# Kernel tuning notes

Measured on AMD Instinct MI355X. Metric: run time of the kernel, lower is better.

## Reference

```python
import jax, jax.numpy as jnp
import numpy as np

V, H, B, T = 32000, 1024, 64, 512
EPS = 1e-5


def setup_inputs() -> dict:
    key = jax.random.key(0)
    ks = jax.random.split(key, 12)
    s = lambda i, shape: (jax.random.normal(ks[i], shape, dtype=jnp.float32) * 0.02)
    inp = {
        "x": jax.random.randint(ks[0], (B, T), 0, V),
        "t": jax.random.uniform(ks[1], (B,), dtype=jnp.float32),
        "emb": s(2, (V, H)),
        "w_ih1": s(3, (4 * H, H)), "w_hh1": s(4, (4 * H, H)),
        "b_ih1": jnp.zeros((4 * H,), jnp.float32), "b_hh1": jnp.zeros((4 * H,), jnp.float32),
        "gamma1": jnp.ones((H,), jnp.float32), "beta1": jnp.zeros((H,), jnp.float32),
        "w_ih2": s(5, (4 * H, H)), "w_hh2": s(6, (4 * H, H)),
        "b_ih2": jnp.zeros((4 * H,), jnp.float32), "b_hh2": jnp.zeros((4 * H,), jnp.float32),
        "gamma2": jnp.ones((H,), jnp.float32), "beta2": jnp.zeros((H,), jnp.float32),
        "fc_w": s(7, (1, H)), "fc_b": jnp.zeros((1,), jnp.float32),
        # LockedDropout: one mask per layer, reused at every timestep, pre-scaled by 1/keep
        "mask1": jax.random.bernoulli(ks[8], 0.5, (B, H)).astype(jnp.float32) / 0.5,
        "mask2": jax.random.bernoulli(ks[9], 0.7, (B, H)).astype(jnp.float32) / 0.7,
    }
    return inp


def _lstm_step(xt, h, c, w_ih, w_hh, b_ih, b_hh):
    # PyTorch LSTMCell gate order: i, f, g, o
    g = xt @ w_ih.T + h @ w_hh.T + (b_ih + b_hh)
    i, f, gg, o = jnp.split(g, 4, axis=-1)
    c = jax.nn.sigmoid(f) * c + jax.nn.sigmoid(i) * jnp.tanh(gg)
    h = jax.nn.sigmoid(o) * jnp.tanh(c)
    return h, c


def _bn(x, gamma, beta):
    # BatchNorm1d in training mode: per-feature batch stats (biased variance)
    m = x.mean(0)
    v = x.var(0)
    return gamma * (x - m) * jax.lax.rsqrt(v + EPS) + beta


def reference(x, t, emb, w_ih1, w_hh1, b_ih1, b_hh1, gamma1, beta1,
              w_ih2, w_hh2, b_ih2, b_hh2, gamma2, beta2, fc_w, fc_b,
              mask1, mask2):
    e = emb[x]                      # [B, T, H]
    e = jnp.transpose(e, (1, 0, 2)) # [T, B, H]

    def step(carry, et):
        h1, c1, h2, c2 = carry
        h1, c1 = _lstm_step(et, h1, c1, w_ih1, w_hh1, b_ih1, b_hh1)
        o = _bn(h1, gamma1, beta1) * mask1
        h2, c2 = _lstm_step(o, h2, c2, w_ih2, w_hh2, b_ih2, b_hh2)
        o = _bn(h2, gamma2, beta2) * mask2
        return (h1, c1, h2, c2), o

    z = jnp.zeros((B, H), jnp.float32)
    _, outs = jax.lax.scan(step, (z, z, z, z), e)  # outs: [T, B, H]

    pooled = outs.max(axis=0)                      # MaxPool1d over time -> [B, H]
    logits = (pooled @ fc_w.T + fc_b)[:, 0]        # [B]
    # BCEWithLogitsLoss (mean), numerically stable
    loss = jnp.mean(jnp.maximum(logits, 0.0) - logits * t + jnp.log1p(jnp.exp(-jnp.abs(logits))))
    return (loss, logits)
```

## Files before the change

### kernel.cpp

```cpp
#include <hip/hip_runtime.h>

#define HDIM  1024
#define BDIM  64
#define TDIM  512
#define FRAGB 131072
#define FRAGE 65536
#define WPAD  1048
#define SLOTS 4
#define NGRP  8

typedef __bf16 bf16x8 __attribute__((ext_vector_type(8)));
typedef float  f32x4  __attribute__((ext_vector_type(4)));
typedef int    i32x4  __attribute__((ext_vector_type(4)));

#define MFMA(a, b, c) __builtin_amdgcn_mfma_f32_16x16x32_bf16(a, b, c, 0, 0, 0)

#define GL(dst, p, off) \
    asm volatile("global_load_dwordx4 %0, %1, off offset:" off " sc0 sc1" \
                 : "=v"(dst) : "v"(p) : "memory")
#define GLF16(f, p) do { \
    const char* p0_ = (const char*)(p); \
    const char* p1_ = p0_ + 4096; const char* p2_ = p0_ + 8192; const char* p3_ = p0_ + 12288; \
    GL(f[0],  p0_, "0"); GL(f[1],  p0_, "1024"); GL(f[2],  p0_, "2048"); GL(f[3],  p0_, "3072"); \
    GL(f[4],  p1_, "0"); GL(f[5],  p1_, "1024"); GL(f[6],  p1_, "2048"); GL(f[7],  p1_, "3072"); \
    GL(f[8],  p2_, "0"); GL(f[9],  p2_, "1024"); GL(f[10], p2_, "2048"); GL(f[11], p2_, "3072"); \
    GL(f[12], p3_, "0"); GL(f[13], p3_, "1024"); GL(f[14], p3_, "2048"); GL(f[15], p3_, "3072"); \
} while (0)
#define WAITV() asm volatile("s_waitcnt vmcnt(0)" ::: "memory")
#define GS16(p, v) \
    asm volatile("global_store_dwordx4 %0, %1, off sc0 sc1" :: "v"(p), "v"(v) : "memory")

__device__ __forceinline__ float sigf(float x) { return 1.0f / (1.0f + expf(-x)); }

__device__ __forceinline__ bf16x8 cvt8(const float* p) {
    const f32x4* q = (const f32x4*)p;
    f32x4 a = q[0], b = q[1];
    bf16x8 r;
    r[0] = (__bf16)a[0]; r[1] = (__bf16)a[1]; r[2] = (__bf16)a[2]; r[3] = (__bf16)a[3];
    r[4] = (__bf16)b[0]; r[5] = (__bf16)b[1]; r[6] = (__bf16)b[2]; r[7] = (__bf16)b[3];
    return r;
}

__device__ __forceinline__ void load16c(bf16x8* f, const char* p) {
#pragma unroll
    for (int i = 0; i < 16; i++) f[i] = *(const bf16x8*)(p + i * 1024);
}

__device__ __forceinline__ void spin2x8(const int* a, const int* b) {
    if (threadIdx.x < 64) {
        int l = threadIdx.x;
        const int* p = nullptr;
        if (l < 8)       { if (a) p = a + l * 16; }
        else if (l < 16) { if (b) p = b + (l - 8) * 16; }
        for (;;) {
            int v = 16;
            if (p) v = __hip_atomic_load(p, __ATOMIC_RELAXED, __HIP_MEMORY_SCOPE_AGENT);
            if (__all(v >= 16)) break;
            __builtin_amdgcn_s_sleep(1);
        }
    }
    __syncthreads();
}
__device__ __forceinline__ void arrive16(int* sub) {
    WAITV();
    __syncthreads();
    if (threadIdx.x == 0)
        __hip_atomic_fetch_add(sub, 1, __ATOMIC_RELAXED, __HIP_MEMORY_SCOPE_AGENT);
}
__device__ __forceinline__ void spin1(const int* c, int n) {
    if (threadIdx.x == 0)
        while (__hip_atomic_load(c, __ATOMIC_RELAXED, __HIP_MEMORY_SCOPE_AGENT) < n)
            __builtin_amdgcn_s_sleep(1);
    __syncthreads();
}

__global__ void gather_emb(const int* __restrict__ x, const float* __restrict__ emb,
                           __bf16* __restrict__ xseqfrag) {
    int t = blockIdx.x;
    for (int u = threadIdx.x; u < 8192; u += 256) {
        int lane = u & 63, c = (u >> 6) & 31, bt = u >> 11;
        int row = lane & 15, quad = lane >> 4;
        int b = bt * 16 + row, k = c * 32 + quad * 8;
        int tok = x[b * TDIM + t];
        bf16x8 r = cvt8(emb + (size_t)tok * HDIM + k);
        *(bf16x8*)(xseqfrag + (size_t)t * FRAGE + (size_t)u * 8) = r;
    }
}

template <int BIG>
__global__ void __launch_bounds__(512, 1) rnn_all(
    const int* __restrict__ x, const float* __restrict__ tv,
    const float* __restrict__ emb,
    const float* __restrict__ w_ih1, const float* __restrict__ w_hh1,
    const float* __restrict__ b_ih1, const float* __restrict__ b_hh1,
    const float* __restrict__ gamma1, const float* __restrict__ beta1,
    const float* __restrict__ w_ih2, const float* __restrict__ w_hh2,
    const float* __restrict__ b_ih2, const float* __restrict__ b_hh2,
    const float* __restrict__ gamma2, const float* __restrict__ beta2,
    const float* __restrict__ fc_w, const float* __restrict__ fc_b,
    const float* __restrict__ mask1, const float* __restrict__ mask2,
    const __bf16* __restrict__ xseq, int use_xseq,
    int* __restrict__ l1s, int* __restrict__ l2s, int* __restrict__ poolg,
    const char* __restrict__ hzero,
    char* __restrict__ h1p, char* __restrict__ h2p, char* __restrict__ o1p,
    float* __restrict__ pooled, float* __restrict__ out) {
    __shared__ __bf16 wih_s[32 * WPAD];
    __shared__ __bf16 whh_s[32 * WPAD];
    __shared__ float bias_s[32];
    __shared__ float gbuf[64 * 36];
    __shared__ float xh[8 * 68];
    __shared__ float stat_m[8], stat_r[8];
    __shared__ __align__(16) __bf16 hstage[512];
    __shared__ __align__(16) __bf16 ostage[512];

    const int tid   = threadIdx.x;
    const int layer = blockIdx.x & 1;
    const int lb    = blockIdx.x >> 1;
    const int grp   = lb >> 4;
    const int fbase = lb * 8;

    const float* w_ih = layer ? w_ih2 : w_ih1;
    const float* w_hh = layer ? w_hh2 : w_hh1;
    const float* b_ih = layer ? b_ih2 : b_ih1;
    const float* b_hh = layer ? b_hh2 : b_hh1;
    const float* gam_ = layer ? gamma2 : gamma1;
    const float* bet_ = layer ? beta2  : beta1;
    const float* msk_ = layer ? mask2  : mask1;

    for (int idx = tid; idx < 32 * HDIM; idx += 512) {
        int n = idx >> 10, k = idx & 1023;
        int row = (n >> 3) * HDIM + fbase + (n & 7);
        wih_s[n * WPAD + k] = (__bf16)w_ih[row * HDIM + k];
        whh_s[n * WPAD + k] = (__bf16)w_hh[row * HDIM + k];
    }
    if (tid < 32) {
        int row = (tid >> 3) * HDIM + fbase + (tid & 7);
        bias_s[tid] = b_ih[row] + b_hh[row];
    }
    __syncthreads();
    if (BIG)
        __builtin_amdgcn_fence(__ATOMIC_ACQUIRE, "agent");

    const int lane = tid & 63;
    const int wv   = tid >> 6;
    const int bt   = wv & 3;
    const int kh   = wv >> 2;
    const int qm   = lane & 15;
    const int quad = lane >> 4;
    const int kbase = kh * 512 + quad * 8;
    const int fragoff = ((bt * 32 + kh * 16) * 64 + lane) * 16;

    const __bf16* bwi0 = wih_s + qm * WPAD + kbase;
    const __bf16* bwi1 = wih_s + (16 + qm) * WPAD + kbase;
    const __bf16* bwh0 = whh_s + qm * WPAD + kbase;
    const __bf16* bwh1 = whh_s + (16 + qm) * WPAD + kbase;

    const int bb = tid >> 3, jj = tid & 7;
    const int feat = fbase + jj;
    const float gv = gam_[feat], bev = bet_[feat], mv = msk_[bb * HDIM + feat];
    float c = 0.0f, pmax = -1e30f;

    const int sbb  = tid & 63;
    const int soff = (((sbb >> 4) * 32 + (lb >> 2)) * 64 + ((lb & 3) * 16 + (sbb & 15))) * 16;

#pragma unroll 1
    for (int t = 0; t < TDIM; t++) {
        f32x4 ax0 = {0.f,0.f,0.f,0.f}, ax1 = {0.f,0.f,0.f,0.f};
        f32x4 ah0 = {0.f,0.f,0.f,0.f}, ah1 = {0.f,0.f,0.f,0.f};
        bf16x8 fh[16];

        if (layer == 0) {
            if (use_xseq) {
                const __bf16* a = xseq + (size_t)t * FRAGE + (fragoff >> 1);
#pragma unroll 4
                for (int i = 0; i < 16; i++) {
                    bf16x8 va = *(const bf16x8*)(a + i * 512);
                    ax0 = MFMA(va, *(const bf16x8*)(bwi0 + i * 32), ax0);
                    ax1 = MFMA(va, *(const bf16x8*)(bwi1 + i * 32), ax1);
                }
            } else {
                const float* a = emb + (size_t)x[(bt * 16 + qm) * TDIM + t] * HDIM + kbase;
#pragma unroll 4
                for (int i = 0; i < 16; i++) {
                    bf16x8 va = cvt8(a + i * 32);
                    ax0 = MFMA(va, *(const bf16x8*)(bwi0 + i * 32), ax0);
                    ax1 = MFMA(va, *(const bf16x8*)(bwi1 + i * 32), ax1);
                }
            }
            if (BIG) {
                spin2x8(t >= 1 ? l1s + (size_t)(t - 1) * NGRP * 16 : nullptr, nullptr);
                const char* src = (t == 0) ? hzero : h1p + (size_t)(t - 1) * FRAGB;
                load16c(fh, src + fragoff);
            } else {
                spin2x8(t >= 1 ? l1s + (size_t)(t - 1) * NGRP * 16 : nullptr,
                        t >= SLOTS ? l2s + (size_t)(t - SLOTS) * NGRP * 16 : nullptr);
                GLF16(fh, h1p + (size_t)(t & 1) * FRAGB + fragoff);
                WAITV();
            }
#pragma unroll
            for (int i = 0; i < 16; i++) {
                ah0 = MFMA(fh[i], *(const bf16x8*)(bwh0 + i * 32), ah0);
                ah1 = MFMA(fh[i], *(const bf16x8*)(bwh1 + i * 32), ah1);
            }
        } else {
            bf16x8 fo[16];
            if (BIG) {
                spin2x8(l1s + (size_t)t * NGRP * 16,
                        t >= 1 ? l2s + (size_t)(t - 1) * NGRP * 16 : nullptr);
                load16c(fo, o1p + (size_t)t * FRAGB + fragoff);
                const char* src = (t == 0) ? hzero : h2p + (size_t)(t - 1) * FRAGB;
                load16c(fh, src + fragoff);
            } else {
                spin2x8(l1s + (size_t)t * NGRP * 16,
                        t >= 1 ? l2s + (size_t)(t - 1) * NGRP * 16 : nullptr);
                GLF16(fo, o1p + (size_t)(t & (SLOTS - 1)) * FRAGB + fragoff);
                GLF16(fh, h2p + (size_t)(t & 1) * FRAGB + fragoff);
                WAITV();
            }
#pragma unroll
            for (int i = 0; i < 16; i++) {
                ax0 = MFMA(fo[i], *(const bf16x8*)(bwi0 + i * 32), ax0);
                ax1 = MFMA(fo[i], *(const bf16x8*)(bwi1 + i * 32), ax1);
                ah0 = MFMA(fh[i], *(const bf16x8*)(bwh0 + i * 32), ah0);
                ah1 = MFMA(fh[i], *(const bf16x8*)(bwh1 + i * 32), ah1);
            }
        }

        if (kh == 0) {
#pragma unroll
            for (int r = 0; r < 4; r++) {
                int row = (bt * 16 + quad * 4 + r) * 36;
                gbuf[row + qm]      = ax0[r] + ah0[r] + bias_s[qm];
                gbuf[row + 16 + qm] = ax1[r] + ah1[r] + bias_s[16 + qm];
            }
        }
        __syncthreads();
        if (kh == 1) {
#pragma unroll
            for (int r = 0; r < 4; r++) {
                int row = (bt * 16 + quad * 4 + r) * 36;
                gbuf[row + qm]      += ax0[r] + ah0[r];
                gbuf[row + 16 + qm] += ax1[r] + ah1[r];
            }
        }
        __syncthreads();

        float gi = gbuf[bb * 36 + jj];
        float gf = gbuf[bb * 36 + 8 + jj];
        float gg = gbuf[bb * 36 + 16 + jj];
        float go = gbuf[bb * 36 + 24 + jj];
        c = sigf(gf) * c + sigf(gi) * tanhf(gg);
        float h = sigf(go) * tanhf(c);
        hstage[tid] = (__bf16)h;
        xh[jj * 68 + bb] = h;
        __syncthreads();
        float v = xh[wv * 68 + lane];
        float s1 = v, s2 = v * v;
#pragma unroll
        for (int off = 32; off; off >>= 1) {
            s1 += __shfl_xor(s1, off);
            s2 += __shfl_xor(s2, off);
        }
        if (lane == 0) {
            float m  = s1 * (1.0f / 64.0f);
            float va = s2 * (1.0f / 64.0f) - m * m;
            stat_m[wv] = m;
            stat_r[wv] = rsqrtf(va + 1e-5f);
        }
        __syncthreads();
        float o = ((h - stat_m[jj]) * stat_r[jj] * gv + bev) * mv;
        if (layer == 0) ostage[tid] = (__bf16)o;
        else            pmax = fmaxf(pmax, o);
        __syncthreads();

        if (layer == 0) {
            size_t hslot = BIG ? (size_t)t * FRAGB : (size_t)((t + 1) & 1) * FRAGB;
            size_t oslot = BIG ? (size_t)t * FRAGB : (size_t)(t & (SLOTS - 1)) * FRAGB;
            if (tid < 64) {
                i32x4 val = *(const i32x4*)(hstage + tid * 8);
                GS16(h1p + hslot + soff, val);
            } else if (tid < 128) {
                i32x4 val = *(const i32x4*)(ostage + (tid - 64) * 8);
                GS16(o1p + oslot + soff, val);
            }
            arrive16(l1s + ((size_t)t * NGRP + grp) * 16);
        } else {
            size_t hslot = BIG ? (size_t)t * FRAGB : (size_t)((t + 1) & 1) * FRAGB;
            if (tid < 64) {
                i32x4 val = *(const i32x4*)(hstage + tid * 8);
                GS16(h2p + hslot + soff, val);
            }
            arrive16(l2s + ((size_t)t * NGRP + grp) * 16);
        }
    }

    if (layer == 1) {
        __hip_atomic_store(&pooled[bb * HDIM + feat], pmax,
                           __ATOMIC_RELAXED, __HIP_MEMORY_SCOPE_AGENT);
        WAITV();
        __syncthreads();
        if (tid == 0)
            __hip_atomic_fetch_add(poolg, 1, __ATOMIC_RELAXED, __HIP_MEMORY_SCOPE_AGENT);

        if (lb == 0) {
            spin1(poolg, 128);
            __builtin_amdgcn_fence(__ATOMIC_ACQUIRE, "agent");
            int b  = wv * 8 + (lane >> 3);
            int l8 = lane & 7;
            float s = 0.0f;
            for (int f = l8 * 128; f < l8 * 128 + 128; f++)
                s += pooled[b * HDIM + f] * fc_w[f];
            s += __shfl_xor(s, 1); s += __shfl_xor(s, 2); s += __shfl_xor(s, 4);
            float logit = s + fc_b[0];
            if (l8 == 0) {
                out[1 + b] = logit;
                gbuf[b] = fmaxf(logit, 0.0f) - logit * tv[b] + log1pf(expf(-fabsf(logit)));
            }
            __syncthreads();
            if (tid < 64) {
                float term = gbuf[tid];
#pragma unroll
                for (int off = 32; off; off >>= 1) term += __shfl_xor(term, off);
                if (tid == 0) out[0] = term * (1.0f / 64.0f);
            }
        }
    }
}

extern "C" void kernel_launch(void* const* d_in, const int* in_sizes, int n_in,
                              void* d_out, int out_size, void* d_ws, size_t ws_size,
                              hipStream_t stream) {
    const int*   x    = (const int*)d_in[0];
    const float* tv   = (const float*)d_in[1];
    const float* emb  = (const float*)d_in[2];
    const float* wih1 = (const float*)d_in[3];
    const float* whh1 = (const float*)d_in[4];
    const float* bih1 = (const float*)d_in[5];
    const float* bhh1 = (const float*)d_in[6];
    const float* g1   = (const float*)d_in[7];
    const float* be1  = (const float*)d_in[8];
    const float* wih2 = (const float*)d_in[9];
    const float* whh2 = (const float*)d_in[10];
    const float* bih2 = (const float*)d_in[11];
    const float* bhh2 = (const float*)d_in[12];
    const float* g2   = (const float*)d_in[13];
    const float* be2  = (const float*)d_in[14];
    const float* fcw  = (const float*)d_in[15];
    const float* fcb  = (const float*)d_in[16];
    const float* m1   = (const float*)d_in[17];
    const float* m2   = (const float*)d_in[18];

    char* w = (char*)d_ws;
    float* out = (float*)d_out;

    const size_t SEQB = (size_t)TDIM * FRAGB;
    size_t boff = 0;
    int*   B_l1s   = (int*)(w + boff); boff += 262144;
    int*   B_l2s   = (int*)(w + boff); boff += 262144;
    int*   B_poolg = (int*)(w + boff); boff += 4096;
    char*  B_hzero = w + boff;         boff += FRAGB;
    size_t B_msz   = boff;
    char*  B_h1    = w + boff;         boff += SEQB;
    char*  B_h2    = w + boff;         boff += SEQB;
    char*  B_o1    = w + boff;         boff += SEQB;
    float* B_pool  = (float*)(w + boff); boff += 262144;
    __bf16* B_xseq = (__bf16*)(w + boff); boff += SEQB;
    size_t need_big = boff;

    if (ws_size >= need_big) {
        hipMemsetAsync(d_ws, 0, B_msz, stream);
        gather_emb<<<dim3(TDIM), dim3(256), 0, stream>>>(x, emb, B_xseq);
        int use_xseq = 1;
        void* args[] = {&x, &tv, &emb, &wih1, &whh1, &bih1, &bhh1, &g1, &be1,
                        &wih2, &whh2, &bih2, &bhh2, &g2, &be2, &fcw, &fcb, &m1, &m2,
                        (void*)&B_xseq, &use_xseq,
                        &B_l1s, &B_l2s, &B_poolg, (void*)&B_hzero,
                        &B_h1, &B_h2, &B_o1, &B_pool, &out};
        hipLaunchCooperativeKernel((void*)rnn_all<1>, dim3(256), dim3(512), args, 0, stream);
        return;
    }

    int*    l1s    = (int*)(w);
    int*    l2s    = (int*)(w + 262144);
    int*    poolg  = (int*)(w + 524288);
    char*   hzero  = w + 524288 + 4096;
    char*   h1frag = w + 528384 + FRAGB;
    char*   h2frag = h1frag + 262144;
    char*   o1frag = h2frag + 262144;
    float*  pooled = (float*)(o1frag + 524288);
    __bf16* xseq   = (__bf16*)((char*)pooled + 262144);
    size_t fixed   = (size_t)((char*)xseq - w);
    int use_xseq = (ws_size >= fixed + SEQB) ? 1 : 0;

    hipMemsetAsync(d_ws, 0, fixed, stream);
    if (use_xseq)
        gather_emb<<<dim3(TDIM), dim3(256), 0, stream>>>(x, emb, xseq);

    void* args[] = {&x, &tv, &emb, &wih1, &whh1, &bih1, &bhh1, &g1, &be1,
                    &wih2, &whh2, &bih2, &bhh2, &g2, &be2, &fcw, &fcb, &m1, &m2,
                    (void*)&xseq, &use_xseq,
                    &l1s, &l2s, &poolg, (void*)&hzero,
                    &h1frag, &h2frag, &o1frag, &pooled, &out};
    hipLaunchCooperativeKernel((void*)rnn_all<0>, dim3(256), dim3(512), args, 0, stream);
}
```

Measured before the change: 4.066 ms.

## Split waves into input and recurrent groups with separate h/o ready flags

Reorganizes each block's 8 waves so half compute the input projection (x or layer-1 output) and half compute the recurrent h projection, each wave covering 32 batch rows with four accumulators. Layer-1 now publishes h and the normalized output through separate counters, so layer-2's input GEMM and layer-1's own recurrence wait only on the data they need. The goal is to take the batchnorm and output store off the recurrent critical path and let the input projection overlap with waiting on the previous h. In exchange it adds more flag arrays and spin points, and the non-BIG path now places hzero at the start of the workspace, overlapping the l1h counters.

```diff
diff --git a/kernel.cpp b/kernel.cpp
--- a/kernel.cpp
+++ b/kernel.cpp
@@ -41,37 +41,44 @@
     return r;
 }
 
-__device__ __forceinline__ void load16c(bf16x8* f, const char* p) {
-#pragma unroll
-    for (int i = 0; i < 16; i++) f[i] = *(const bf16x8*)(p + i * 1024);
-}
-
-__device__ __forceinline__ void spin2x8(const int* a, const int* b) {
-    if (threadIdx.x < 64) {
-        int l = threadIdx.x;
-        const int* p = nullptr;
-        if (l < 8)       { if (a) p = a + l * 16; }
-        else if (l < 16) { if (b) p = b + (l - 8) * 16; }
-        for (;;) {
-            int v = 16;
-            if (p) v = __hip_atomic_load(p, __ATOMIC_RELAXED, __HIP_MEMORY_SCOPE_AGENT);
-            if (__all(v >= 16)) break;
-            __builtin_amdgcn_s_sleep(1);
-        }
-    }
-    __syncthreads();
-}
-__device__ __forceinline__ void arrive16(int* sub) {
-    WAITV();
-    __syncthreads();
-    if (threadIdx.x == 0)
-        __hip_atomic_fetch_add(sub, 1, __ATOMIC_RELAXED, __HIP_MEMORY_SCOPE_AGENT);
+__device__ __forceinline__ void wspin(const int* base) {
+    int l = threadIdx.x & 63;
+    const int* p = (l < 8) ? base + l * 16 : nullptr;
+    for (;;) {
+        int v = p ? __hip_atomic_load(p, __ATOMIC_RELAXED, __HIP_MEMORY_SCOPE_AGENT) : 16;
+        if (__all(v >= 16)) break;
+        __builtin_amdgcn_s_sleep(1);
+    }
 }
 __device__ __forceinline__ void spin1(const int* c, int n) {
     if (threadIdx.x == 0)
         while (__hip_atomic_load(c, __ATOMIC_RELAXED, __HIP_MEMORY_SCOPE_AGENT) < n)
             __builtin_amdgcn_s_sleep(1);
     __syncthreads();
+}
+
+__device__ __forceinline__ void gemm16(const char* pa, const __bf16* bw0, const __bf16* bw1,
+                                       f32x4& c00, f32x4& c01, f32x4& c10, f32x4& c11) {
+#pragma unroll
+    for (int i = 0; i < 16; i++) {
+        bf16x8 a0v = *(const bf16x8*)(pa + i * 1024);
+        bf16x8 a1v = *(const bf16x8*)(pa + 32768 + i * 1024);
+        bf16x8 w0  = *(const bf16x8*)(bw0 + i * 32);
+        bf16x8 w1  = *(const bf16x8*)(bw1 + i * 32);
+        c00 = MFMA(a0v, w0, c00); c01 = MFMA(a0v, w1, c01);
+        c10 = MFMA(a1v, w0, c10); c11 = MFMA(a1v, w1, c11);
+    }
+}
+__device__ __forceinline__ void gemm16s(const bf16x8* f0, const bf16x8* f1,
+                                        const __bf16* bw0, const __bf16* bw1,
+                                        f32x4& c00, f32x4& c01, f32x4& c10, f32x4& c11) {
+#pragma unroll
+    for (int i = 0; i < 16; i++) {
+        bf16x8 w0 = *(const bf16x8*)(bw0 + i * 32);
+        bf16x8 w1 = *(const bf16x8*)(bw1 + i * 32);
+        c00 = MFMA(f0[i], w0, c00); c01 = MFMA(f0[i], w1, c01);
+        c10 = MFMA(f1[i], w0, c10); c11 = MFMA(f1[i], w1, c11);
+    }
 }
 
 __global__ void gather_emb(const int* __restrict__ x, const float* __restrict__ emb,
@@ -100,14 +107,15 @@
     const float* __restrict__ fc_w, const float* __restrict__ fc_b,
     const float* __restrict__ mask1, const float* __restrict__ mask2,
     const __bf16* __restrict__ xseq, int use_xseq,
-    int* __restrict__ l1s, int* __restrict__ l2s, int* __restrict__ poolg,
-    const char* __restrict__ hzero,
+    int* __restrict__ l1h, int* __restrict__ l1o, int* __restrict__ l2h,
+    int* __restrict__ poolg, const char* __restrict__ hzero,
     char* __restrict__ h1p, char* __restrict__ h2p, char* __restrict__ o1p,
     float* __restrict__ pooled, float* __restrict__ out) {
     __shared__ __bf16 wih_s[32 * WPAD];
     __shared__ __bf16 whh_s[32 * WPAD];
     __shared__ float bias_s[32];
-    __shared__ float gbuf[64 * 36];
+    __shared__ float gbufX[32 * 68];
+    __shared__ float gbufH[32 * 68];
     __shared__ float xh[8 * 68];
     __shared__ float stat_m[8], stat_r[8];
     __shared__ __align__(16) __bf16 hstage[512];
@@ -143,117 +151,112 @@
 
     const int lane = tid & 63;
     const int wv   = tid >> 6;
-    const int bt   = wv & 3;
-    const int kh   = wv >> 2;
+    const int bh   = wv & 1;
+    const int kh   = (wv >> 1) & 1;
+    const int g    = wv >> 2;
     const int qm   = lane & 15;
     const int quad = lane >> 4;
-    const int kbase = kh * 512 + quad * 8;
-    const int fragoff = ((bt * 32 + kh * 16) * 64 + lane) * 16;
-
-    const __bf16* bwi0 = wih_s + qm * WPAD + kbase;
-    const __bf16* bwi1 = wih_s + (16 + qm) * WPAD + kbase;
-    const __bf16* bwh0 = whh_s + qm * WPAD + kbase;
-    const __bf16* bwh1 = whh_s + (16 + qm) * WPAD + kbase;
+    const int aoff = (bh * 64 + kh * 16) * 1024 + lane * 16;
+
+    const __bf16* bw0 = (g ? whh_s : wih_s) + qm * WPAD + kh * 512 + quad * 8;
+    const __bf16* bw1 = bw0 + 16 * WPAD;
 
     const int bb = tid >> 3, jj = tid & 7;
     const int feat = fbase + jj;
     const float gv = gam_[feat], bev = bet_[feat], mv = msk_[bb * HDIM + feat];
-    float c = 0.0f, pmax = -1e30f;
-
-    const int sbb  = tid & 63;
-    const int soff = (((sbb >> 4) * 32 + (lb >> 2)) * 64 + ((lb & 3) * 16 + (sbb & 15))) * 16;
+    float cst = 0.0f, pmax = -1e30f;
+
+    const int soff = (((lane >> 4) * 32 + (lb >> 2)) * 64 + ((lb & 3) * 16 + (lane & 15))) * 16;
+
+    char* h_self = layer ? h2p : h1p;
+    int*  ch     = layer ? l2h : l1h;
 
 #pragma unroll 1
     for (int t = 0; t < TDIM; t++) {
-        f32x4 ax0 = {0.f,0.f,0.f,0.f}, ax1 = {0.f,0.f,0.f,0.f};
-        f32x4 ah0 = {0.f,0.f,0.f,0.f}, ah1 = {0.f,0.f,0.f,0.f};
-        bf16x8 fh[16];
-
-        if (layer == 0) {
-            if (use_xseq) {
-                const __bf16* a = xseq + (size_t)t * FRAGE + (fragoff >> 1);
+        f32x4 a00 = {0.f,0.f,0.f,0.f}, a01 = {0.f,0.f,0.f,0.f};
+        f32x4 a10 = {0.f,0.f,0.f,0.f}, a11 = {0.f,0.f,0.f,0.f};
+
+        if (g == 0) {
+            if (layer == 0) {
+                if (use_xseq) {
+                    gemm16((const char*)xseq + (size_t)t * FRAGB + aoff, bw0, bw1,
+                           a00, a01, a10, a11);
+                } else {
+                    const float* pe0 = emb + (size_t)x[(bh*32 + qm)*TDIM + t]*HDIM + kh*512 + quad*8;
+                    const float* pe1 = emb + (size_t)x[(bh*32 + 16 + qm)*TDIM + t]*HDIM + kh*512 + quad*8;
 #pragma unroll 4
-                for (int i = 0; i < 16; i++) {
-                    bf16x8 va = *(const bf16x8*)(a + i * 512);
-                    ax0 = MFMA(va, *(const bf16x8*)(bwi0 + i * 32), ax0);
-                    ax1 = MFMA(va, *(const bf16x8*)(bwi1 + i * 32), ax1);
+                    for (int i = 0; i < 16; i++) {
+                        bf16x8 v0 = cvt8(pe0 + i * 32), v1 = cvt8(pe1 + i * 32);
+                        bf16x8 w0 = *(const bf16x8*)(bw0 + i * 32);
+                        bf16x8 w1 = *(const bf16x8*)(bw1 + i * 32);
+                        a00 = MFMA(v0, w0, a00); a01 = MFMA(v0, w1, a01);
+                        a10 = MFMA(v1, w0, a10); a11 = MFMA(v1, w1, a11);
+                    }
                 }
             } else {
-                const float* a = emb + (size_t)x[(bt * 16 + qm) * TDIM + t] * HDIM + kbase;
-#pragma unroll 4
-                for (int i = 0; i < 16; i++) {
-                    bf16x8 va = cvt8(a + i * 32);
-                    ax0 = MFMA(va, *(const bf16x8*)(bwi0 + i * 32), ax0);
-                    ax1 = MFMA(va, *(const bf16x8*)(bwi1 + i * 32), ax1);
+                wspin(l1o + (size_t)t * NGRP * 16);
+                if (BIG) {
+                    gemm16(o1p + (size_t)t * FRAGB + aoff, bw0, bw1, a00, a01, a10, a11);
+                } else {
+                    bf16x8 f0[16], f1[16];
+                    const char* p = o1p + (size_t)(t & (SLOTS - 1)) * FRAGB + aoff;
+                    GLF16(f0, p); GLF16(f1, p + 32768); WAITV();
+                    gemm16s(f0, f1, bw0, bw1, a00, a01, a10, a11);
                 }
             }
+        } else {
+            if (t >= 1) wspin(ch + (size_t)(t - 1) * NGRP * 16);
             if (BIG) {
-                spin2x8(t >= 1 ? l1s + (size_t)(t - 1) * NGRP * 16 : nullptr, nullptr);
-                const char* src = (t == 0) ? hzero : h1p + (size_t)(t - 1) * FRAGB;
-                load16c(fh, src + fragoff);
+                const char* src = (t == 0) ? hzero : (const char*)(h_self + (size_t)(t - 1) * FRAGB);
+                gemm16(src + aoff, bw0, bw1, a00, a01, a10, a11);
             } else {
-                spin2x8(t >= 1 ? l1s + (size_t)(t - 1) * NGRP * 16 : nullptr,
-                        t >= SLOTS ? l2s + (size_t)(t - SLOTS) * NGRP * 16 : nullptr);
-                GLF16(fh, h1p + (size_t)(t & 1) * FRAGB + fragoff);
-                WAITV();
-            }
-#pragma unroll
-            for (int i = 0; i < 16; i++) {
-                ah0 = MFMA(fh[i], *(const bf16x8*)(bwh0 + i * 32), ah0);
-                ah1 = MFMA(fh[i], *(const bf16x8*)(bwh1 + i * 32), ah1);
-            }
-        } else {
-            bf16x8 fo[16];
-            if (BIG) {
-                spin2x8(l1s + (size_t)t * NGRP * 16,
-                        t >= 1 ? l2s + (size_t)(t - 1) * NGRP * 16 : nullptr);
-                load16c(fo, o1p + (size_t)t * FRAGB + fragoff);
-                const char* src = (t == 0) ? hzero : h2p + (size_t)(t - 1) * FRAGB;
-                load16c(fh, src + fragoff);
-            } else {
-                spin2x8(l1s + (size_t)t * NGRP * 16,
-                        t >= 1 ? l2s + (size_t)(t - 1) * NGRP * 16 : nullptr);
-                GLF16(fo, o1p + (size_t)(t & (SLOTS - 1)) * FRAGB + fragoff);
-                GLF16(fh, h2p + (size_t)(t & 1) * FRAGB + fragoff);
-                WAITV();
-            }
-#pragma unroll
-            for (int i = 0; i < 16; i++) {
-                ax0 = MFMA(fo[i], *(const bf16x8*)(bwi0 + i * 32), ax0);
-                ax1 = MFMA(fo[i], *(const bf16x8*)(bwi1 + i * 32), ax1);
-                ah0 = MFMA(fh[i], *(const bf16x8*)(bwh0 + i * 32), ah0);
-                ah1 = MFMA(fh[i], *(const bf16x8*)(bwh1 + i * 32), ah1);
-            }
-        }
-
+                bf16x8 f0[16], f1[16];
+                const char* p = h_self + (size_t)(t & 1) * FRAGB + aoff;
+                GLF16(f0, p); GLF16(f1, p + 32768); WAITV();
+                gemm16s(f0, f1, bw0, bw1, a00, a01, a10, a11);
+            }
+        }
+
+        float* myg = g ? gbufH : gbufX;
+        const int r0  = bh * 32 + quad * 4;
+        const int i00 = qm * 68 + r0, i01 = (16 + qm) * 68 + r0;
         if (kh == 0) {
-#pragma unroll
-            for (int r = 0; r < 4; r++) {
-                int row = (bt * 16 + quad * 4 + r) * 36;
-                gbuf[row + qm]      = ax0[r] + ah0[r] + bias_s[qm];
-                gbuf[row + 16 + qm] = ax1[r] + ah1[r] + bias_s[16 + qm];
-            }
+            if (!g) {
+                float b0 = bias_s[qm], b1 = bias_s[16 + qm];
+                f32x4 s0 = {b0, b0, b0, b0}, s1 = {b1, b1, b1, b1};
+                a00 += s0; a01 += s1; a10 += s0; a11 += s1;
+            }
+            *(f32x4*)&myg[i00]      = a00;
+            *(f32x4*)&myg[i01]      = a01;
+            *(f32x4*)&myg[i00 + 16] = a10;
+            *(f32x4*)&myg[i01 + 16] = a11;
         }
         __syncthreads();
         if (kh == 1) {
-#pragma unroll
-            for (int r = 0; r < 4; r++) {
-                int row = (bt * 16 + quad * 4 + r) * 36;
-                gbuf[row + qm]      += ax0[r] + ah0[r];
-                gbuf[row + 16 + qm] += ax1[r] + ah1[r];
-            }
+            f32x4 v;
+            v = *(const f32x4*)&myg[i00];      v += a00; *(f32x4*)&myg[i00]      = v;
+            v = *(const f32x4*)&myg[i01];      v += a01; *(f32x4*)&myg[i01]      = v;
+            v = *(const f32x4*)&myg[i00 + 16]; v += a10; *(f32x4*)&myg[i00 + 16] = v;
+            v = *(const f32x4*)&myg[i01 + 16]; v += a11; *(f32x4*)&myg[i01 + 16] = v;
         }
         __syncthreads();
 
-        float gi = gbuf[bb * 36 + jj];
-        float gf = gbuf[bb * 36 + 8 + jj];
-        float gg = gbuf[bb * 36 + 16 + jj];
-        float go = gbuf[bb * 36 + 24 + jj];
-        c = sigf(gf) * c + sigf(gi) * tanhf(gg);
-        float h = sigf(go) * tanhf(c);
+        const int cb = jj * 68 + bb;
+        float gi = gbufX[cb]          + gbufH[cb];
+        float gf = gbufX[cb + 8*68]   + gbufH[cb + 8*68];
+        float gg = gbufX[cb + 16*68]  + gbufH[cb + 16*68];
+        float go = gbufX[cb + 24*68]  + gbufH[cb + 24*68];
+        cst = sigf(gf) * cst + sigf(gi) * tanhf(gg);
+        float h = sigf(go) * tanhf(cst);
         hstage[tid] = (__bf16)h;
         xh[jj * 68 + bb] = h;
         __syncthreads();
+
+        size_t hslot = BIG ? (size_t)t * FRAGB : (size_t)((t + 1) & 1) * FRAGB;
+        if (wv == 0) {
+            i32x4 val = *(const i32x4*)(hstage + lane * 8);
+            GS16(h_self + hslot + soff, val);
+        }
         float v = xh[wv * 68 + lane];
         float s1 = v, s2 = v * v;
 #pragma unroll
@@ -267,30 +270,31 @@
             stat_m[wv] = m;
             stat_r[wv] = rsqrtf(va + 1e-5f);
         }
+        if (wv == 0) {
+            WAITV();
+            if (lane == 0)
+                __hip_atomic_fetch_add(ch + ((size_t)t * NGRP + grp) * 16, 1,
+                                       __ATOMIC_RELAXED, __HIP_MEMORY_SCOPE_AGENT);
+        }
         __syncthreads();
+
         float o = ((h - stat_m[jj]) * stat_r[jj] * gv + bev) * mv;
-        if (layer == 0) ostage[tid] = (__bf16)o;
-        else            pmax = fmaxf(pmax, o);
-        __syncthreads();
-
         if (layer == 0) {
-            size_t hslot = BIG ? (size_t)t * FRAGB : (size_t)((t + 1) & 1) * FRAGB;
-            size_t oslot = BIG ? (size_t)t * FRAGB : (size_t)(t & (SLOTS - 1)) * FRAGB;
-            if (tid < 64) {
-                i32x4 val = *(const i32x4*)(hstage + tid * 8);
-                GS16(h1p + hslot + soff, val);
-            } else if (tid < 128) {
-                i32x4 val = *(const i32x4*)(ostage + (tid - 64) * 8);
+            ostage[tid] = (__bf16)o;
+            __syncthreads();
+            if (wv == 1) {
+                if (!BIG && t >= SLOTS)
+                    wspin(l2h + (size_t)(t - SLOTS) * NGRP * 16);
+                i32x4 val = *(const i32x4*)(ostage + lane * 8);
+                size_t oslot = BIG ? (size_t)t * FRAGB : (size_t)(t & (SLOTS - 1)) * FRAGB;
                 GS16(o1p + oslot + soff, val);
-            }
-            arrive16(l1s + ((size_t)t * NGRP + grp) * 16);
+                WAITV();
+                if (lane == 0)
+                    __hip_atomic_fetch_add(l1o + ((size_t)t * NGRP + grp) * 16, 1,
+                                           __ATOMIC_RELAXED, __HIP_MEMORY_SCOPE_AGENT);
+            }
         } else {
-            size_t hslot = BIG ? (size_t)t * FRAGB : (size_t)((t + 1) & 1) * FRAGB;
-            if (tid < 64) {
-                i32x4 val = *(const i32x4*)(hstage + tid * 8);
-                GS16(h2p + hslot + soff, val);
-            }
-            arrive16(l2s + ((size_t)t * NGRP + grp) * 16);
+            pmax = fmaxf(pmax, o);
         }
     }
 
@@ -314,11 +318,11 @@
             float logit = s + fc_b[0];
             if (l8 == 0) {
                 out[1 + b] = logit;
-                gbuf[b] = fmaxf(logit, 0.0f) - logit * tv[b] + log1pf(expf(-fabsf(logit)));
+                gbufX[b] = fmaxf(logit, 0.0f) - logit * tv[b] + log1pf(expf(-fabsf(logit)));
             }
             __syncthreads();
             if (tid < 64) {
-                float term = gbuf[tid];
+                float term = gbufX[tid];
 #pragma unroll
                 for (int off = 32; off; off >>= 1) term += __shfl_xor(term, off);
                 if (tid == 0) out[0] = term * (1.0f / 64.0f);
@@ -355,8 +359,9 @@
 
     const size_t SEQB = (size_t)TDIM * FRAGB;
     size_t boff = 0;
-    int*   B_l1s   = (int*)(w + boff); boff += 262144;
-    int*   B_l2s   = (int*)(w + boff); boff += 262144;
+    int*   B_l1h   = (int*)(w + boff); boff += 262144;
+    int*   B_l1o   = (int*)(w + boff); boff += 262144;
+    int*   B_l2h   = (int*)(w + boff); boff += 262144;
     int*   B_poolg = (int*)(w + boff); boff += 4096;
     char*  B_hzero = w + boff;         boff += FRAGB;
     size_t B_msz   = boff;
@@ -374,17 +379,18 @@
         void* args[] = {&x, &tv, &emb, &wih1, &whh1, &bih1, &bhh1, &g1, &be1,
                         &wih2, &whh2, &bih2, &bhh2, &g2, &be2, &fcw, &fcb, &m1, &m2,
                         (void*)&B_xseq, &use_xseq,
-                        &B_l1s, &B_l2s, &B_poolg, (void*)&B_hzero,
+                        &B_l1h, &B_l1o, &B_l2h, &B_poolg, (void*)&B_hzero,
                         &B_h1, &B_h2, &B_o1, &B_pool, &out};
         hipLaunchCooperativeKernel((void*)rnn_all<1>, dim3(256), dim3(512), args, 0, stream);
         return;
     }
 
-    int*    l1s    = (int*)(w);
-    int*    l2s    = (int*)(w + 262144);
-    int*    poolg  = (int*)(w + 524288);
-    char*   hzero  = w + 524288 + 4096;
-    char*   h1frag = w + 528384 + FRAGB;
+    int*    l1h    = (int*)(w);
+    int*    l1o    = (int*)(w + 262144);
+    int*    l2h    = (int*)(w + 524288);
+    int*    poolg  = (int*)(w + 786432);
+    char*   hzero  = w;
+    char*   h1frag = w + 790528;
     char*   h2frag = h1frag + 262144;
     char*   o1frag = h2frag + 262144;
     float*  pooled = (float*)(o1frag + 524288);
@@ -399,7 +405,7 @@
     void* args[] = {&x, &tv, &emb, &wih1, &whh1, &bih1, &bhh1, &g1, &be1,
                     &wih2, &whh2, &bih2, &bhh2, &g2, &be2, &fcw, &fcb, &m1, &m2,
                     (void*)&xseq, &use_xseq,
-                    &l1s, &l2s, &poolg, (void*)&hzero,
+                    &l1h, &l1o, &l2h, &poolg, (void*)&hzero,
                     &h1frag, &h2frag, &o1frag, &pooled, &out};
     hipLaunchCooperativeKernel((void*)rnn_all<0>, dim3(256), dim3(512), args, 0, stream);
 }
```

Measured after the change: 3.908 ms. 3.9% less time.
